# Kernel optimization log

Hardware: AMD Instinct MI355X
Metric: run time of the kernel (lower is better)

Reference implementation:

```python
import jax, jax.numpy as jnp
import numpy as np
from jax import lax

K = 5          # dynamic kernel size
GROUPS = 8     # inter_channels // group_channels = 128 // 16
R = 2          # pixel shuffle upscale factor
SLOPE = 0.01   # LeakyReLU default negative_slope
EPS = 1e-5     # BatchNorm eps


def conv2d(x, w, b, pad=0):
    # x: [B,C,H,W], w: [O,I,kh,kw]
    y = lax.conv_general_dilated(x, w, (1, 1), [(pad, pad), (pad, pad)],
                                 dimension_numbers=('NCHW', 'OIHW', 'NCHW'))
    return y + b[None, :, None, None]


def pixel_shuffle(x, r):
    B, C, H, W = x.shape
    x = x.reshape(B, C // (r * r), r, r, H, W)
    x = x.transpose(0, 1, 4, 2, 5, 3)  # B, C', H, r, W, r
    return x.reshape(B, C // (r * r), H * r, W * r)


def involution(x, weight, k, groups, pad):
    # x: [B,C,H,W]; weight: [B,groups,k,k,H,W]
    # out[b, g*gc+c, h, w] = sum_ij weight[b,g,i,j,h,w] * x_pad[b, g*gc+c, h+i, w+j]
    B, C, H, W = x.shape
    gc = C // groups
    xp = jnp.pad(x, ((0, 0), (0, 0), (pad, pad), (pad, pad)))
    xg = xp.reshape(B, groups, gc, H + 2 * pad, W + 2 * pad)
    out = jnp.zeros((B, groups, gc, H, W), x.dtype)
    for i in range(k):
        for j in range(k):
            out = out + weight[:, :, None, i, j] * xg[:, :, :, i:i + H, j:j + W]
    return out.reshape(B, C, H, W)


def setup_inputs() -> dict:
    key = jax.random.key(0)
    ks = jax.random.split(key, 16)
    s = 0.05
    return {
        'high_level': jax.random.normal(ks[0], (8, 128, 64, 64), jnp.float32),
        'low_level': jax.random.normal(ks[1], (8, 224, 128, 128), jnp.float32),
        'emb': jax.random.normal(ks[2], (8, 256, 128, 128), jnp.float32),
        'reduce_w': jax.random.normal(ks[3], (128, 256, 1, 1), jnp.float32) * s,
        'reduce_b': jax.random.normal(ks[4], (128,), jnp.float32) * s,
        'conv1_w': jax.random.normal(ks[5], (32, 128, 1, 1), jnp.float32) * s,
        'conv1_b': jax.random.normal(ks[6], (32,), jnp.float32) * s,
        'conv2_w': jax.random.normal(ks[7], (200, 32, 3, 3), jnp.float32) * s,
        'conv2_b': jax.random.normal(ks[8], (200,), jnp.float32) * s,
        'embconv_w': jax.random.normal(ks[9], (32, 256, 1, 1), jnp.float32) * s,
        'embconv_b': jax.random.normal(ks[10], (32,), jnp.float32) * s,
        'out_w': jax.random.normal(ks[11], (64, 128, 1, 1), jnp.float32) * s,
        'out_b': jax.random.normal(ks[12], (64,), jnp.float32) * s,
        'bn_gamma': jnp.ones((64,), jnp.float32),
        'bn_beta': jnp.zeros((64,), jnp.float32),
        'bn_mean': jnp.zeros((64,), jnp.float32),
        'bn_var': jax.random.uniform(ks[13], (64,), jnp.float32, 0.5, 1.5),
    }


def reference(high_level, low_level, emb,
              reduce_w, reduce_b, conv1_w, conv1_b, conv2_w, conv2_b,
              embconv_w, embconv_b, out_w, out_b,
              bn_gamma, bn_beta, bn_mean, bn_var):
    cat = jnp.concatenate([pixel_shuffle(high_level, R), low_level], axis=1)
    cat = conv2d(cat, reduce_w, reduce_b)
    mix = jax.nn.leaky_relu(conv2d(cat, conv1_w, conv1_b)
                            + conv2d(emb, embconv_w, embconv_b), SLOPE)
    w = conv2d(mix, conv2_w, conv2_b, pad=1)  # [B, K*K*GROUPS, H, W]
    B, _, H, W = w.shape
    w = w.reshape(B, GROUPS, K, K, H, W)
    o = involution(cat, w, K, GROUPS, (K - 1) // 2)
    o = conv2d(o, out_w, out_b)
    o = (o - bn_mean[None, :, None, None]) * (bn_gamma[None, :, None, None]
        / jnp.sqrt(bn_var[None, :, None, None] + EPS)) + bn_beta[None, :, None, None]
    return jax.nn.leaky_relu(o, SLOPE)
```

## Files before the change

kernel.cpp:

```cpp
#include <hip/hip_runtime.h>

typedef unsigned short u16; typedef unsigned int u32; typedef unsigned long long u64;
typedef __attribute__((ext_vector_type(8))) short short8;
typedef __attribute__((ext_vector_type(16))) float f32x16;

#define HW 16384

#define RED_B  0
#define C1E_B  128
#define C2_B   160
#define OUT_B  416
#define BN_SC  480
#define BN_SH  544
#define FLAG_OFF   4096
#define RWB_OFF    8192
#define C1B_OFF    73728
#define EMBB_OFF   81920
#define OUTB_OFF   98304
#define C2PB_OFF   114688
#define CAT2_OFF   524288
#define MIX_OFF    34078720
#define WGT_OFF    42467328

__device__ __forceinline__ float bf2f(u16 x){ u32 u=((u32)x)<<16; float f; __builtin_memcpy(&f,&u,4); return f; }
__device__ __forceinline__ u16 f2bf(float f){ u32 u; __builtin_memcpy(&u,&f,4); return (u16)((u + 0x7fffu + ((u>>16)&1u))>>16); }
__device__ __forceinline__ float lrelu(float x){ return x>0.f ? x : 0.01f*x; }

template<int M> __device__ __forceinline__ u16 ldb(const void* p, size_t i){
    if (M==1) return ((const u16*)p)[i];
    return f2bf(((const float*)p)[i]);
}
template<int M> __device__ __forceinline__ float ldf(const void* p, size_t i){
    if (M==1) return bf2f(((const u16*)p)[i]);
    return ((const float*)p)[i];
}
template<int M> __device__ __forceinline__ short8 ld8(const void* p, size_t i){
    short8 v;
    if (M==1){ __builtin_memcpy(&v, (const u16*)p + i, 16); }
    else {
        float a[8]; __builtin_memcpy(a, (const float*)p + i, 32);
#pragma unroll
        for (int r=0;r<8;r++) v[r] = (short)f2bf(a[r]);
    }
    return v;
}
__device__ __forceinline__ void stA(u16* At, int stride, int p, int c, u16 v){
    At[p*stride + ((((c>>3) ^ ((p>>1)&7)))<<3) + (c&7)] = v;
}

__global__ void detect_kernel(const void* __restrict__ emb, u32* __restrict__ flag){
    int tid = threadIdx.x;
    const u16* p = (const u16*)emb;
    int e = (p[tid*2] >> 7) & 0xFF;
    u64 m = __ballot(e >= 100 && e <= 140);
    if (tid == 0) *flag = (__popcll(m) >= 32) ? 1u : 0u;
}

template<int M>
__global__ __launch_bounds__(256) void k_prep(
    const void* rw, const void* rb, const void* c1w, const void* c1b,
    const void* c2w, const void* c2b, const void* ew, const void* eb,
    const void* ow, const void* ob, const void* gam, const void* bet,
    const void* mn, const void* vr, char* ws, const u32* flag)
{
    if (*flag != (u32)M) return;
    float* wf = (float*)ws;
    int i = blockIdx.x*256 + threadIdx.x;
    if (i < 32768)       ((u16*)(ws+RWB_OFF))[i] = ldb<M>(rw, i);
    else if (i < 36864)  ((u16*)(ws+C1B_OFF))[i-32768] = ldb<M>(c1w, i-32768);
    else if (i < 45056)  ((u16*)(ws+EMBB_OFF))[i-36864] = ldb<M>(ew, i-36864);
    else if (i < 53248)  ((u16*)(ws+OUTB_OFF))[i-45056] = ldb<M>(ow, i-45056);
    else if (i < 126976) {
        int j = i-53248; int o = j/288, k = j - o*288;
        int tap = k>>5, ic = k&31;
        u16 v = 0;
        if (o < 200) v = ldb<M>(c2w, (size_t)o*288 + ic*9 + tap);
        ((u16*)(ws+C2PB_OFF))[j] = v;
    }
    else if (i < 127584) {
        int j = i-126976;
        if (j < 128) wf[RED_B+j] = ldf<M>(rb, j);
        else if (j < 160) wf[C1E_B+j-128] = ldf<M>(c1b, j-128) + ldf<M>(eb, j-128);
        else if (j < 416) { int o = j-160; wf[C2_B+o] = (o<200) ? ldf<M>(c2b,o) : 0.f; }
        else if (j < 480) wf[OUT_B+j-416] = ldf<M>(ob, j-416);
        else if (j < 544) { int c=j-480; wf[BN_SC+c] = ldf<M>(gam,c) * rsqrtf(ldf<M>(vr,c)+1e-5f); }
        else { int c=j-544; wf[BN_SH+c] = ldf<M>(bet,c) - ldf<M>(mn,c)*ldf<M>(gam,c)*rsqrtf(ldf<M>(vr,c)+1e-5f); }
    }
}

template<int M>
__global__ __launch_bounds__(256) void k_reduce(
    const void* __restrict__ hi, const void* __restrict__ lo,
    const u16* __restrict__ rwB, const float* __restrict__ wf,
    u16* __restrict__ cat2, const u32* __restrict__ flag)
{
    if (*flag != (u32)M) return;
    __shared__ u16 At[64*264];
    const int tid = threadIdx.x, wvi = tid>>6, lane = tid&63;
    const int rt = (wvi>>1)*32, nc0 = (wvi&1)*64;
    const int col = lane&31, q = lane>>5;

    const int gpx = blockIdx.x*64;
    const int b = gpx>>14, p0 = gpx&16383;
    const int h = p0>>7, w0 = p0&127;

    short8 B[2][16];
#pragma unroll
    for (int nt=0; nt<2; nt++){
        int o = nc0 + nt*32 + col;
#pragma unroll
        for (int s=0; s<16; s++)
            __builtin_memcpy(&B[nt][s], rwB + (size_t)o*256 + s*16 + q*8, 16);
    }

    if (tid < 224) {
        int c = tid;
        size_t base = ((size_t)(b*224 + c))*HW + p0;
#pragma unroll
        for (int i=0;i<8;i++){
            short8 v = ld8<M>(lo, base + 8*i);
#pragma unroll
            for (int j=0;j<8;j++) stA(At,264, 8*i+j, 32+c, (u16)v[j]);
        }
    } else {
        int cc = tid - 224;
        int hc = cc*4 + (h&1)*2;
        size_t srcE = ((size_t)(b*128 + hc))*4096 + (size_t)(h>>1)*64 + (w0>>1);
#pragma unroll
        for (int i=0;i<4;i++){
            short8 e = ld8<M>(hi, srcE + 8*i);
            short8 o = ld8<M>(hi, srcE + 4096 + 8*i);
#pragma unroll
            for (int j=0;j<8;j++){
                stA(At,264, 16*i+2*j,   cc, (u16)e[j]);
                stA(At,264, 16*i+2*j+1, cc, (u16)o[j]);
            }
        }
    }
    __syncthreads();

    f32x16 acc0, acc1;
#pragma unroll
    for (int r=0;r<16;r++){ acc0[r]=0.f; acc1[r]=0.f; }
    int pp = rt + col, sw = (pp>>1)&7;
    const u16* arow = At + pp*264;
#pragma unroll
    for (int s=0;s<16;s++){
        short8 a;
        __builtin_memcpy(&a, arow + (((2*s+q)^sw)<<3), 16);
        acc0 = __builtin_amdgcn_mfma_f32_32x32x16_bf16(a, B[0][s], acc0, 0,0,0);
        acc1 = __builtin_amdgcn_mfma_f32_32x32x16_bf16(a, B[1][s], acc1, 0,0,0);
    }
#pragma unroll
    for (int nt=0; nt<2; nt++){
        int oc = nc0 + nt*32 + col;
        float bias = wf[RED_B + oc];
#pragma unroll
        for (int r=0;r<16;r++){
            int row = (r&3) + 8*(r>>2) + 4*q;
            float v = (nt ? acc1[r] : acc0[r]) + bias;
            cat2[((size_t)(gpx + rt + row))*128 + oc] = f2bf(v);
        }
    }
}

template<int M>
__global__ __launch_bounds__(256) void k_mix(
    const u16* __restrict__ cat2, const void* __restrict__ emb,
    const u16* __restrict__ c1B, const u16* __restrict__ embB,
    const float* __restrict__ wf, u16* __restrict__ mixt, const u32* __restrict__ flag)
{
    if (*flag != (u32)M) return;
    __shared__ u16 At[128*136];
    const int tid = threadIdx.x, wvi = tid>>6, lane = tid&63;
    const int rt = wvi*32, col = lane&31, q = lane>>5;

    const int gpx = blockIdx.x*128;
    const int b = gpx>>14, p0 = gpx&16383;

    short8 Bc[8];
#pragma unroll
    for (int s=0;s<8;s++)  __builtin_memcpy(&Bc[s], c1B + (size_t)col*128 + s*16 + q*8, 16);

    f32x16 acc;
#pragma unroll
    for (int r=0;r<16;r++) acc[r]=0.f;
    int pp = rt + col, sw = (pp>>1)&7;
    const u16* arow = At + pp*136;

#pragma unroll
    for (int i=0;i<8;i++){
        int idx = tid + i*256;
        int p = idx>>4, c16 = idx&15;
        short8 v;
        __builtin_memcpy(&v, cat2 + ((size_t)(gpx+p))*128 + c16*8, 16);
        *(short8*)(At + p*136 + ((c16 ^ ((p>>1)&7))<<3)) = v;
    }
    __syncthreads();
#pragma unroll
    for (int s=0;s<8;s++){
        short8 a; __builtin_memcpy(&a, arow + (((2*s+q)^sw)<<3), 16);
        acc = __builtin_amdgcn_mfma_f32_32x32x16_bf16(a, Bc[s], acc, 0,0,0);
    }

    const int chalf = (wvi&1)*64, pxh = (wvi>>1)*64;
#pragma unroll 1
    for (int half=0; half<2; half++){
        short8 Be[8];
#pragma unroll
        for (int s=0;s<8;s++)
            __builtin_memcpy(&Be[s], embB + (size_t)col*256 + half*128 + s*16 + q*8, 16);
        __syncthreads();
        {
            int c = half*128 + chalf + lane;
            int cl = chalf + lane;
            size_t base = ((size_t)(b*256 + c))*HW + p0 + pxh;
#pragma unroll
            for (int i=0;i<8;i++){
                short8 v = ld8<M>(emb, base + 8*i);
#pragma unroll
                for (int j=0;j<8;j++) stA(At,136, pxh+8*i+j, cl, (u16)v[j]);
            }
        }
        __syncthreads();
#pragma unroll
        for (int s=0;s<8;s++){
            short8 a; __builtin_memcpy(&a, arow + (((2*s+q)^sw)<<3), 16);
            acc = __builtin_amdgcn_mfma_f32_32x32x16_bf16(a, Be[s], acc, 0,0,0);
        }
    }
    float bias = wf[C1E_B + col];
#pragma unroll
    for (int r=0;r<16;r++){
        int row = (r&3) + 8*(r>>2) + 4*q;
        mixt[((size_t)(gpx + rt + row))*32 + col] = f2bf(lrelu(acc[r] + bias));
    }
}

__global__ __launch_bounds__(256) void k_conv2(
    const u16* __restrict__ mixt, const u16* __restrict__ c2B,
    const float* __restrict__ wf, u16* __restrict__ wgt)
{
    __shared__ u16 halo[100*32];
    const int tid = threadIdx.x, wvi = tid>>6, lane = tid&63;
    const int rt = (wvi>>1)*32, npair = wvi&1;
    const int nh = blockIdx.x & 1;
    const int nc0 = nh*128 + npair*64;
    const int col = lane&31, q = lane>>5;

    short8 B[2][18];
#pragma unroll
    for (int nt=0; nt<2; nt++){
        int o = nc0 + nt*32 + col;
#pragma unroll
        for (int s=0; s<18; s++)
            __builtin_memcpy(&B[nt][s], c2B + (size_t)o*288 + s*16 + q*8, 16);
    }

    for (int it=0; it<4; it++){
        int tile = (blockIdx.x>>1) + it*512;
        int b = tile>>8, tl = tile&255;
        int ty = tl>>4, tx = tl&15;
        __syncthreads();
#pragma unroll
        for (int i=0;i<2;i++){
            int idx = tid + i*256;
            if (idx < 400){
                int point = idx>>2, cq = idx&3;
                int y = ty*8 + point/10 - 1, x = tx*8 + point%10 - 1;
                short8 v;
                if (y>=0 && y<128 && x>=0 && x<128)
                    __builtin_memcpy(&v, mixt + ((size_t)(b*HW + y*128 + x))*32 + cq*8, 16);
                else { short z = 0; v = (short8){z,z,z,z,z,z,z,z}; }
                *(short8*)(halo + point*32 + cq*8) = v;
            }
        }
        __syncthreads();

        f32x16 acc0, acc1;
#pragma unroll
        for (int r=0;r<16;r++){ acc0[r]=0.f; acc1[r]=0.f; }
        int pp = rt + col, py = pp>>3, px = pp&7;
#pragma unroll
        for (int s=0;s<18;s++){
            int tap = s>>1, ih = s&1;
            int dy = tap/3, dx = tap%3;
            short8 a;
            __builtin_memcpy(&a, halo + ((py+dy)*10 + px+dx)*32 + ih*16 + q*8, 16);
            acc0 = __builtin_amdgcn_mfma_f32_32x32x16_bf16(a, B[0][s], acc0, 0,0,0);
            acc1 = __builtin_amdgcn_mfma_f32_32x32x16_bf16(a, B[1][s], acc1, 0,0,0);
        }
#pragma unroll
        for (int nt=0; nt<2; nt++){
            int oc = nc0 + nt*32 + col;
            if (oc < 200){
                float bias = wf[C2_B + oc];
#pragma unroll
                for (int r=0;r<16;r++){
                    int row = (r&3) + 8*(r>>2) + 4*q;
                    int p2 = rt + row;
                    int y = ty*8 + (p2>>3), x = tx*8 + (p2&7);
                    float v = (nt ? acc1[r] : acc0[r]) + bias;
                    wgt[((size_t)(b*200 + oc))*HW + y*128 + x] = f2bf(v);
                }
            }
        }
    }
}

template<int M>
__global__ __launch_bounds__(256) void k_inv(
    const u16* __restrict__ cat2, const u16* __restrict__ wgt,
    const u16* __restrict__ outB, const float* __restrict__ wf,
    void* __restrict__ out, const u32* __restrict__ flag)
{
    if (*flag != (u32)M) return;
    __shared__ u16 halo[400*16];
    __shared__ u16 og[256*16];
    const int tid = threadIdx.x, wvi = tid>>6, lane = tid&63;
    const int col = lane&31, q = lane>>5;
    const int b = blockIdx.y, ty = blockIdx.x>>3, tx = blockIdx.x&7;
    const int py = tid>>4, px = tid&15;
    const int h = ty*16 + py, w = tx*16 + px;

    f32x16 acc[2][2];
#pragma unroll
    for (int i=0;i<2;i++)
#pragma unroll
    for (int j=0;j<2;j++)
#pragma unroll
    for (int r=0;r<16;r++) acc[i][j][r] = 0.f;

#pragma unroll 1
    for (int g=0; g<8; g++){
        __syncthreads();
#pragma unroll
        for (int i=0;i<4;i++){
            int idx = tid + i*256;
            if (idx < 800){
                int point = idx>>1, cq = idx&1;
                int y = ty*16 + point/20 - 2, x = tx*16 + point%20 - 2;
                short8 v;
                if (y>=0 && y<128 && x>=0 && x<128)
                    __builtin_memcpy(&v, cat2 + ((size_t)(b*HW + y*128 + x))*128 + g*16 + cq*8, 16);
                else { short z=0; v = (short8){z,z,z,z,z,z,z,z}; }
                *(short8*)(halo + point*16 + cq*8) = v;
            }
        }
        __syncthreads();

        float wvv[25];
#pragma unroll
        for (int t=0;t<25;t++)
            wvv[t] = bf2f(wgt[((size_t)(b*200 + g*25 + t))*HW + h*128 + w]);

        float a16[16];
#pragma unroll
        for (int cc=0;cc<16;cc++) a16[cc]=0.f;
#pragma unroll
        for (int t=0;t<25;t++){
            int dy = t/5, dx = t%5;
            u32 vv[8];
            __builtin_memcpy(vv, halo + ((py+dy)*20 + px+dx)*16, 32);
            float wt = wvv[t];
#pragma unroll
            for (int r=0;r<8;r++){
                u32 u = vv[r];
                u32 ulo = u<<16, uhi = u & 0xffff0000u;
                float x0, x1;
                __builtin_memcpy(&x0,&ulo,4); __builtin_memcpy(&x1,&uhi,4);
                a16[2*r]   += wt*x0;
                a16[2*r+1] += wt*x1;
            }
        }
        u32 pk[8];
#pragma unroll
        for (int r=0;r<8;r++) pk[r] = (u32)f2bf(a16[2*r]) | ((u32)f2bf(a16[2*r+1])<<16);
        __syncthreads();
        __builtin_memcpy(og + tid*16, pk, 32);
        __syncthreads();

        short8 bo0, bo1;
        __builtin_memcpy(&bo0, outB + (size_t)(col)*128      + g*16 + q*8, 16);
        __builtin_memcpy(&bo1, outB + (size_t)(32+col)*128   + g*16 + q*8, 16);
#pragma unroll
        for (int rt2=0; rt2<2; rt2++){
            int prow = (wvi*2 + rt2)*32 + col;
            short8 a; __builtin_memcpy(&a, og + prow*16 + q*8, 16);
            acc[rt2][0] = __builtin_amdgcn_mfma_f32_32x32x16_bf16(a, bo0, acc[rt2][0], 0,0,0);
            acc[rt2][1] = __builtin_amdgcn_mfma_f32_32x32x16_bf16(a, bo1, acc[rt2][1], 0,0,0);
        }
    }
#pragma unroll
    for (int rt2=0; rt2<2; rt2++)
#pragma unroll
    for (int nt=0; nt<2; nt++){
        int oc = nt*32 + col;
        float bias = wf[OUT_B+oc], sc = wf[BN_SC+oc], sh = wf[BN_SH+oc];
#pragma unroll
        for (int r=0;r<16;r++){
            int row = (r&3) + 8*(r>>2) + 4*q;
            int p = (wvi*2 + rt2)*32 + row;
            int yy = ty*16 + (p>>4), xx = tx*16 + (p&15);
            float v = lrelu((acc[rt2][nt][r] + bias)*sc + sh);
            size_t oidx = ((size_t)(b*64 + oc))*HW + yy*128 + xx;
            if (M==1) ((u16*)out)[oidx] = f2bf(v);
            else ((float*)out)[oidx] = v;
        }
    }
}

extern "C" void kernel_launch(void* const* d_in, const int* in_sizes, int n_in,
                              void* d_out, int out_size, void* d_ws, size_t ws_size,
                              hipStream_t stream) {
    const void* hi  = d_in[0];
    const void* lo  = d_in[1];
    const void* emb = d_in[2];
    char* ws = (char*)d_ws;
    float* wf = (float*)ws;
    u32* flag = (u32*)(ws + FLAG_OFF);
    u16* cat2 = (u16*)(ws + CAT2_OFF);
    u16* mixt = (u16*)(ws + MIX_OFF);
    u16* wgt  = (u16*)(ws + WGT_OFF);

    detect_kernel<<<1, 64, 0, stream>>>(emb, flag);

    k_prep<0><<<499,256,0,stream>>>(d_in[3],d_in[4],d_in[5],d_in[6],d_in[7],d_in[8],
        d_in[9],d_in[10],d_in[11],d_in[12],d_in[13],d_in[14],d_in[15],d_in[16], ws, flag);
    k_prep<1><<<499,256,0,stream>>>(d_in[3],d_in[4],d_in[5],d_in[6],d_in[7],d_in[8],
        d_in[9],d_in[10],d_in[11],d_in[12],d_in[13],d_in[14],d_in[15],d_in[16], ws, flag);

    k_reduce<0><<<2048,256,0,stream>>>(hi, lo, (const u16*)(ws+RWB_OFF), wf, cat2, flag);
    k_reduce<1><<<2048,256,0,stream>>>(hi, lo, (const u16*)d_in[3],      wf, cat2, flag);

    k_mix<0><<<1024,256,0,stream>>>(cat2, emb, (const u16*)(ws+C1B_OFF), (const u16*)(ws+EMBB_OFF), wf, mixt, flag);
    k_mix<1><<<1024,256,0,stream>>>(cat2, emb, (const u16*)d_in[5],      (const u16*)d_in[9],       wf, mixt, flag);

    k_conv2<<<1024,256,0,stream>>>(mixt, (const u16*)(ws+C2PB_OFF), wf, wgt);

    k_inv<0><<<dim3(64,8),256,0,stream>>>(cat2, wgt, (const u16*)(ws+OUTB_OFF), wf, d_out, flag);
    k_inv<1><<<dim3(64,8),256,0,stream>>>(cat2, wgt, (const u16*)d_in[11],      wf, d_out, flag);
}
```

Measured before the change: 476.8 us.

## Vectorize reduce-kernel LDS staging and pre-swizzle reduce weights for coalesced loads

The reduce kernel's input staging changes from scalar per-element LDS stores to an in-register 8x8 transpose, with each thread writing 16-byte chunks under a new swizzle function. The prep kernel rewrites the reduce weight matrix into an MFMA-fragment-major layout, so each lane loads its B fragments with contiguous coalesced 16-byte reads. Those B loads move after the LDS fill and are split into two halves to lower register pressure. The bf16 path now also uses the reordered workspace weights, so it depends on k_prep having run.

Result: faster. 462.2 us (-3.1%).

```diff
diff --git a/kernel.cpp b/kernel.cpp
--- a/kernel.cpp
+++ b/kernel.cpp
@@ -44,9 +44,18 @@
     }
     return v;
 }
+template<int M> __device__ __forceinline__ void ld4(const void* p, size_t i, u32* d){
+    if (M==1){ __builtin_memcpy(d, (const u16*)p + i, 8); }
+    else {
+        float a[4]; __builtin_memcpy(a, (const float*)p + i, 16);
+        d[0] = (u32)f2bf(a[0]) | ((u32)f2bf(a[1])<<16);
+        d[1] = (u32)f2bf(a[2]) | ((u32)f2bf(a[3])<<16);
+    }
+}
 __device__ __forceinline__ void stA(u16* At, int stride, int p, int c, u16 v){
     At[p*stride + ((((c>>3) ^ ((p>>1)&7)))<<3) + (c&7)] = v;
 }
+__device__ __forceinline__ int swz(int p){ return ((p>>1) ^ (p>>3)) & 7; }
 
 __global__ void detect_kernel(const void* __restrict__ emb, u32* __restrict__ flag){
     int tid = threadIdx.x;
@@ -66,7 +75,12 @@
     if (*flag != (u32)M) return;
     float* wf = (float*)ws;
     int i = blockIdx.x*256 + threadIdx.x;
-    if (i < 32768)       ((u16*)(ws+RWB_OFF))[i] = ldb<M>(rw, i);
+    if (i < 32768) {
+        int o = i>>8, ic = i&255;
+        int s = ic>>4, qq = (ic>>3)&1, e = ic&7;
+        int dst = (((o>>5)*16 + s)*64 + qq*32 + (o&31))*8 + e;
+        ((u16*)(ws+RWB_OFF))[dst] = ldb<M>(rw, i);
+    }
     else if (i < 36864)  ((u16*)(ws+C1B_OFF))[i-32768] = ldb<M>(c1w, i-32768);
     else if (i < 45056)  ((u16*)(ws+EMBB_OFF))[i-36864] = ldb<M>(ew, i-36864);
     else if (i < 53248)  ((u16*)(ws+OUTB_OFF))[i-45056] = ldb<M>(ow, i-45056);
@@ -104,53 +118,94 @@
     const int b = gpx>>14, p0 = gpx&16383;
     const int h = p0>>7, w0 = p0&127;
 
-    short8 B[2][16];
-#pragma unroll
-    for (int nt=0; nt<2; nt++){
-        int o = nc0 + nt*32 + col;
-#pragma unroll
-        for (int s=0; s<16; s++)
-            __builtin_memcpy(&B[nt][s], rwB + (size_t)o*256 + s*16 + q*8, 16);
-    }
-
-    if (tid < 224) {
-        int c = tid;
-        size_t base = ((size_t)(b*224 + c))*HW + p0;
-#pragma unroll
-        for (int i=0;i<8;i++){
-            short8 v = ld8<M>(lo, base + 8*i);
-#pragma unroll
-            for (int j=0;j<8;j++) stA(At,264, 8*i+j, 32+c, (u16)v[j]);
+    const int co = tid>>3, po = tid&7;
+    u32 W[8][4];
+    if (co < 28) {
+        u32 R[8][4];
+#pragma unroll
+        for (int j=0;j<8;j++){
+            short8 v = ld8<M>(lo, ((size_t)(b*224 + 8*co + j))*HW + p0 + 8*po);
+            __builtin_memcpy(&R[j][0], &v, 16);
+        }
+#pragma unroll
+        for (int p=0;p<8;p++){
+            const int u = p>>1, hf = p&1;
+#pragma unroll
+            for (int m=0;m<4;m++){
+                u32 A0 = R[2*m][u], A1 = R[2*m+1][u];
+                W[p][m] = hf ? ((A0>>16) | (A1 & 0xffff0000u))
+                             : ((A0 & 0xffffu) | (A1<<16));
+            }
+        }
+        const int ch = co + 4;
+#pragma unroll
+        for (int p=0;p<8;p++){
+            int pg = 8*po + p;
+            __builtin_memcpy(At + pg*264 + ((ch ^ swz(pg))<<3), &W[p][0], 16);
         }
     } else {
-        int cc = tid - 224;
-        int hc = cc*4 + (h&1)*2;
-        size_t srcE = ((size_t)(b*128 + hc))*4096 + (size_t)(h>>1)*64 + (w0>>1);
-#pragma unroll
-        for (int i=0;i<4;i++){
-            short8 e = ld8<M>(hi, srcE + 8*i);
-            short8 o = ld8<M>(hi, srcE + 4096 + 8*i);
-#pragma unroll
-            for (int j=0;j<8;j++){
-                stA(At,264, 16*i+2*j,   cc, (u16)e[j]);
-                stA(At,264, 16*i+2*j+1, cc, (u16)o[j]);
-            }
+        const int cc0 = (co-28)*8, h2 = (h&1)*2;
+        u32 E[8][2], O[8][2];
+#pragma unroll
+        for (int j=0;j<8;j++){
+            int hc = (cc0+j)*4 + h2;
+            size_t src = ((size_t)(b*128 + hc))*4096 + (size_t)(h>>1)*64 + (w0>>1) + 4*po;
+            ld4<M>(hi, src,        E[j]);
+            ld4<M>(hi, src + 4096, O[j]);
+        }
+#pragma unroll
+        for (int p=0;p<8;p++){
+            const int k = p>>1, u = k>>1, hf = k&1;
+#pragma unroll
+            for (int m=0;m<4;m++){
+                u32 A0, A1;
+                if (p&1){ A0 = O[2*m][u]; A1 = O[2*m+1][u]; }
+                else    { A0 = E[2*m][u]; A1 = E[2*m+1][u]; }
+                W[p][m] = hf ? ((A0>>16) | (A1 & 0xffff0000u))
+                             : ((A0 & 0xffffu) | (A1<<16));
+            }
+        }
+        const int ch = co - 28;
+#pragma unroll
+        for (int p=0;p<8;p++){
+            int pg = 8*po + p;
+            __builtin_memcpy(At + pg*264 + ((ch ^ swz(pg))<<3), &W[p][0], 16);
         }
     }
     __syncthreads();
 
+    const int pp = rt + col, sw = swz(pp);
+    const u16* arow = At + pp*264;
+    const int ot0 = (wvi&1)*2;
+
     f32x16 acc0, acc1;
 #pragma unroll
     for (int r=0;r<16;r++){ acc0[r]=0.f; acc1[r]=0.f; }
-    int pp = rt + col, sw = (pp>>1)&7;
-    const u16* arow = At + pp*264;
-#pragma unroll
-    for (int s=0;s<16;s++){
-        short8 a;
-        __builtin_memcpy(&a, arow + (((2*s+q)^sw)<<3), 16);
-        acc0 = __builtin_amdgcn_mfma_f32_32x32x16_bf16(a, B[0][s], acc0, 0,0,0);
-        acc1 = __builtin_amdgcn_mfma_f32_32x32x16_bf16(a, B[1][s], acc1, 0,0,0);
-    }
+
+    short8 Bb[2][8];
+#pragma unroll
+    for (int nt=0;nt<2;nt++)
+#pragma unroll
+    for (int s=0;s<8;s++)
+        __builtin_memcpy(&Bb[nt][s], rwB + (((size_t)((ot0+nt)*16 + s))*64 + lane)*8, 16);
+#pragma unroll
+    for (int s=0;s<8;s++){
+        short8 a; __builtin_memcpy(&a, arow + (((2*s+q)^sw)<<3), 16);
+        acc0 = __builtin_amdgcn_mfma_f32_32x32x16_bf16(a, Bb[0][s], acc0, 0,0,0);
+        acc1 = __builtin_amdgcn_mfma_f32_32x32x16_bf16(a, Bb[1][s], acc1, 0,0,0);
+    }
+#pragma unroll
+    for (int nt=0;nt<2;nt++)
+#pragma unroll
+    for (int s=0;s<8;s++)
+        __builtin_memcpy(&Bb[nt][s], rwB + (((size_t)((ot0+nt)*16 + 8+s))*64 + lane)*8, 16);
+#pragma unroll
+    for (int s=8;s<16;s++){
+        short8 a; __builtin_memcpy(&a, arow + (((2*s+q)^sw)<<3), 16);
+        acc0 = __builtin_amdgcn_mfma_f32_32x32x16_bf16(a, Bb[0][s-8], acc0, 0,0,0);
+        acc1 = __builtin_amdgcn_mfma_f32_32x32x16_bf16(a, Bb[1][s-8], acc1, 0,0,0);
+    }
+
 #pragma unroll
     for (int nt=0; nt<2; nt++){
         int oc = nc0 + nt*32 + col;
@@ -431,7 +486,7 @@
         d_in[9],d_in[10],d_in[11],d_in[12],d_in[13],d_in[14],d_in[15],d_in[16], ws, flag);
 
     k_reduce<0><<<2048,256,0,stream>>>(hi, lo, (const u16*)(ws+RWB_OFF), wf, cat2, flag);
-    k_reduce<1><<<2048,256,0,stream>>>(hi, lo, (const u16*)d_in[3],      wf, cat2, flag);
+    k_reduce<1><<<2048,256,0,stream>>>(hi, lo, (const u16*)(ws+RWB_OFF), wf, cat2, flag);
 
     k_mix<0><<<1024,256,0,stream>>>(cat2, emb, (const u16*)(ws+C1B_OFF), (const u16*)(ws+EMBB_OFF), wf, mixt, flag);
     k_mix<1><<<1024,256,0,stream>>>(cat2, emb, (const u16*)d_in[5],      (const u16*)d_in[9],       wf, mixt, flag);
```
